# Optimization experiments

Measured on AMD Instinct MI355X. Metric: run time of the kernel, lower is better.

The kernel has to match this reference:

```python
import jax, jax.numpy as jnp
import numpy as np

K = 7  # hardcoded pooling grid in the module


def setup_inputs() -> dict:
    key = jax.random.key(0)
    k1, k2, k3, k4, k5 = jax.random.split(key, 5)
    B, C1, H, W = 4, 21, 100, 100
    cls_conv_out = jax.random.normal(k1, (B, C1 * K * K, H, W), dtype=jnp.float32)
    n = 2000
    # ROIs: (ymin, xmin, ymax, xmax) integer coords; spans >= K so bin steps >= 1
    ymin = jax.random.randint(k2, (n,), 0, 40)
    ylen = jax.random.randint(k3, (n,), K, 57)
    xmin = jax.random.randint(k4, (n,), 0, 40)
    xlen = jax.random.randint(k5, (n,), K, 57)
    rois = jnp.stack([ymin, xmin, ymin + ylen, xmin + xlen], axis=1).astype(jnp.int32)
    return {"cls_conv_out": cls_conv_out, "rois": rois}


def _ps_roi_pool(cls_conv_out, rois):
    k = K
    B, C, H, W = cls_conv_out.shape
    c1 = C // (k * k)
    # Original indexes batch element `_ - 1` where `_` is the batch size -> last element.
    # Channel ordering from the `count` counter: channel = (j*k + l)*c1 + cls.
    feat = cls_conv_out[B - 1].reshape(k, k, c1, H, W)
    # Integral image (summed-area table) so each variable-size bin mean is 4 gathers.
    I = jnp.pad(feat, ((0, 0), (0, 0), (0, 0), (1, 0), (1, 0))).cumsum(axis=3).cumsum(axis=4)  # [k,k,c1,H+1,W+1]

    ymin, xmin, ymax, xmax = rois[:, 0], rois[:, 1], rois[:, 2], rois[:, 3]
    ys = (ymax - ymin) // k  # per-ROI bin step (int floor, as in int(range/k))
    xs = (xmax - xmin) // k
    j = jnp.arange(k)
    y0 = ymin[:, None] + j[None, :] * ys[:, None]  # [n,k] bin starts
    y1 = y0 + ys[:, None]                          # [n,k] bin stops
    x0 = xmin[:, None] + j[None, :] * xs[:, None]
    x1 = x0 + xs[:, None]

    jj = j[None, :, None, None]
    ll = j[None, None, :, None]
    cc = jnp.arange(c1)[None, None, None, :]
    Y0 = y0[:, :, None, None]; Y1 = y1[:, :, None, None]
    X0 = x0[:, None, :, None]; X1 = x1[:, None, :, None]
    # bin sums via SAT: [n, k, k, c1]
    S = (I[jj, ll, cc, Y1, X1] - I[jj, ll, cc, Y0, X1]
         - I[jj, ll, cc, Y1, X0] + I[jj, ll, cc,0*Y0 + Y0, X0])
    area = (ys * xs).astype(S.dtype)[:, None, None, None]
    pooled = S / area  # per-bin mean -> pooling_track, layout [n,k,k,c1]
    return pooled


def reference(cls_conv_out, rois):
    pooled = _ps_roi_pool(cls_conv_out, rois)          # [n,k,k,c1]
    avg = pooled.mean(axis=(1, 2))                     # AvgPool2d((7,7)) -> [n,c1]
    # nn.Softmax() on a 4D tensor applies over dim=1 (classes)
    scores = jax.nn.softmax(avg, axis=1)[:, :, None, None]  # [n,c1,1,1]
    return scores
```

## Files before the change

### kernel.cpp

```cpp
#include <hip/hip_runtime.h>
#include <math.h>

#define KK      7
#define C1      21
#define NPLANES (KK * KK * C1)
#define H       100
#define W       100

__global__ __launch_bounds__(256) void plane_partial(
    const float* __restrict__ src,
    size_t batch_off,
    const int*  __restrict__ rois,
    int nrois,
    float* __restrict__ partial)
{
    const int p  = blockIdx.x;
    const int c  = p % C1;           (void)c;
    const int jl = p / C1;
    const int l  = jl % KK;
    const int j  = jl / KK;
    const int t  = threadIdx.x;

    __shared__ float tile[H * W];

    const float* plane = src + batch_off + (size_t)p * (H * W);
    for (int i = t; i < H * W; i += blockDim.x) tile[i] = plane[i];
    __syncthreads();

    if (t < H) {
        float s = 0.f;
        int base = t * W;
        for (int x = 0; x < W; ++x) { s += tile[base + x]; tile[base + x] = s; }
    }
    __syncthreads();

    if (t < W) {
        float s = 0.f;
        for (int y = 0; y < H; ++y) { s += tile[y * W + t]; tile[y * W + t] = s; }
    }
    __syncthreads();

    for (int n = t; n < nrois; n += blockDim.x) {
        const int4 r  = ((const int4*)rois)[n];
        const int ys  = (r.z - r.x) / KK;
        const int xs  = (r.w - r.y) / KK;
        const int y0  = r.x + j * ys;
        const int x0  = r.y + l * xs;
        const int y1  = y0 + ys - 1;
        const int x1  = x0 + xs - 1;

        float S = tile[y1 * W + x1];
        if (x0 > 0)           S -= tile[y1 * W + (x0 - 1)];
        if (y0 > 0)           S -= tile[(y0 - 1) * W + x1];
        if (y0 > 0 && x0 > 0) S += tile[(y0 - 1) * W + (x0 - 1)];

        partial[(size_t)n * NPLANES + p] = S;
    }
}

__global__ __launch_bounds__(256) void reduce_softmax(
    const float* __restrict__ partial,
    const int*   __restrict__ rois,
    float*       __restrict__ out)
{
    const int n = blockIdx.x;
    const int t = threadIdx.x;

    __shared__ float chsum[C1];
    if (t < C1) chsum[t] = 0.f;
    __syncthreads();

    const float* pp = partial + (size_t)n * NPLANES;
    for (int idx = t; idx < NPLANES; idx += blockDim.x) {
        atomicAdd(&chsum[idx % C1], pp[idx]);
    }
    __syncthreads();

    if (t == 0) {
        const int4 r  = ((const int4*)rois)[n];
        const int ys  = (r.z - r.x) / KK;
        const int xs  = (r.w - r.y) / KK;
        const float inv = 1.0f / (49.0f * (float)(ys * xs));

        float m = -INFINITY;
        float v[C1];
        for (int c = 0; c < C1; ++c) { v[c] = chsum[c] * inv; m = fmaxf(m, v[c]); }
        float s = 0.f;
        for (int c = 0; c < C1; ++c) { v[c] = expf(v[c] - m); s += v[c]; }
        const float rs = 1.0f / s;
        for (int c = 0; c < C1; ++c) out[(size_t)n * C1 + c] = v[c] * rs;
    }
}

__global__ __launch_bounds__(256) void roi_pool_direct(
    const float* __restrict__ src,
    size_t batch_off,
    const int*   __restrict__ rois,
    float*       __restrict__ out)
{
    const int n = blockIdx.x;
    const int t = threadIdx.x;

    __shared__ float chsum[C1];
    if (t < C1) chsum[t] = 0.f;
    __syncthreads();

    const int ymin = rois[4 * n + 0];
    const int xmin = rois[4 * n + 1];
    const int ymax = rois[4 * n + 2];
    const int xmax = rois[4 * n + 3];
    const int ys = (ymax - ymin) / KK;
    const int xs = (xmax - xmin) / KK;

    const float* base = src + batch_off;

    for (int idx = t; idx < NPLANES; idx += blockDim.x) {
        const int c  = idx % C1;
        const int jl = idx / C1;
        const int l  = jl % KK;
        const int j  = jl / KK;
        const int y0 = ymin + j * ys;
        const int x0 = xmin + l * xs;
        const float* plane = base + (size_t)idx * (H * W);
        float s = 0.f;
        for (int y = y0; y < y0 + ys; ++y) {
            const float* row = plane + (size_t)y * W + x0;
            for (int x = 0; x < xs; ++x) s += row[x];
        }
        atomicAdd(&chsum[c], s);
    }
    __syncthreads();

    if (t == 0) {
        const float inv = 1.0f / (49.0f * (float)(ys * xs));
        float m = -INFINITY;
        float v[C1];
        for (int c = 0; c < C1; ++c) { v[c] = chsum[c] * inv; m = fmaxf(m, v[c]); }
        float s = 0.f;
        for (int c = 0; c < C1; ++c) { v[c] = expf(v[c] - m); s += v[c]; }
        const float rs = 1.0f / s;
        for (int c = 0; c < C1; ++c) out[(size_t)n * C1 + c] = v[c] * rs;
    }
}

extern "C" void kernel_launch(void* const* d_in, const int* in_sizes, int n_in,
                              void* d_out, int out_size, void* d_ws, size_t ws_size,
                              hipStream_t stream)
{
    const float* cls  = (const float*)d_in[0];
    const int*   rois = (const int*)d_in[1];
    float*       out  = (float*)d_out;

    const int nrois = in_sizes[1] / 4;
    const size_t plane_elems = (size_t)NPLANES * H * W;
    const int B = (int)((size_t)in_sizes[0] / plane_elems);
    const size_t batch_off = (size_t)(B - 1) * plane_elems;

    const size_t need = (size_t)nrois * NPLANES * sizeof(float);
    if (ws_size >= need) {
        float* partial = (float*)d_ws;
        plane_partial<<<NPLANES, 256, 0, stream>>>(cls, batch_off, rois, nrois, partial);
        reduce_softmax<<<nrois, 256, 0, stream>>>(partial, rois, out);
    } else {
        roi_pool_direct<<<nrois, 256, 0, stream>>>(cls, batch_off, rois, out);
    }
}
```

Measured before the change: 266.3 us.

## Accumulate per-class bin sums with global atomics instead of a full partial buffer

```diff
diff --git a/kernel.cpp b/kernel.cpp
--- a/kernel.cpp
+++ b/kernel.cpp
@@ -7,15 +7,21 @@
 #define H       100
 #define W       100
 
-__global__ __launch_bounds__(256) void plane_partial(
+__global__ __launch_bounds__(256) void zero_acc(float* __restrict__ acc, int n)
+{
+    int i = blockIdx.x * 256 + threadIdx.x;
+    if (i < n) acc[i] = 0.f;
+}
+
+__global__ __launch_bounds__(256) void plane_accum(
     const float* __restrict__ src,
     size_t batch_off,
     const int*  __restrict__ rois,
     int nrois,
-    float* __restrict__ partial)
+    float* __restrict__ acc)
 {
     const int p  = blockIdx.x;
-    const int c  = p % C1;           (void)c;
+    const int c  = p % C1;
     const int jl = p / C1;
     const int l  = jl % KK;
     const int j  = jl / KK;
@@ -23,8 +29,11 @@
 
     __shared__ float tile[H * W];
 
-    const float* plane = src + batch_off + (size_t)p * (H * W);
-    for (int i = t; i < H * W; i += blockDim.x) tile[i] = plane[i];
+    {
+        const float4* p4 = (const float4*)(src + batch_off + (size_t)p * (H * W));
+        float4* t4 = (float4*)tile;
+        for (int i = t; i < (H * W) / 4; i += 256) t4[i] = p4[i];
+    }
     __syncthreads();
 
     if (t < H) {
@@ -40,7 +49,7 @@
     }
     __syncthreads();
 
-    for (int n = t; n < nrois; n += blockDim.x) {
+    for (int n = t; n < nrois; n += 256) {
         const int4 r  = ((const int4*)rois)[n];
         const int ys  = (r.z - r.x) / KK;
         const int xs  = (r.w - r.y) / KK;
@@ -54,42 +63,37 @@
         if (y0 > 0)           S -= tile[(y0 - 1) * W + x1];
         if (y0 > 0 && x0 > 0) S += tile[(y0 - 1) * W + (x0 - 1)];
 
-        partial[(size_t)n * NPLANES + p] = S;
+        atomicAdd(&acc[(size_t)n * C1 + c], S);
     }
 }
 
-__global__ __launch_bounds__(256) void reduce_softmax(
-    const float* __restrict__ partial,
+__global__ __launch_bounds__(256) void softmax_out(
+    const float* __restrict__ acc,
     const int*   __restrict__ rois,
+    int nrois,
     float*       __restrict__ out)
 {
-    const int n = blockIdx.x;
-    const int t = threadIdx.x;
+    const int n = blockIdx.x * 256 + threadIdx.x;
+    if (n >= nrois) return;
 
-    __shared__ float chsum[C1];
-    if (t < C1) chsum[t] = 0.f;
-    __syncthreads();
+    const int4 r  = ((const int4*)rois)[n];
+    const int ys  = (r.z - r.x) / KK;
+    const int xs  = (r.w - r.y) / KK;
+    const float inv = 1.0f / (49.0f * (float)(ys * xs));
 
-    const float* pp = partial + (size_t)n * NPLANES;
-    for (int idx = t; idx < NPLANES; idx += blockDim.x) {
-        atomicAdd(&chsum[idx % C1], pp[idx]);
+    float v[C1];
+    float m = -INFINITY;
+    #pragma unroll
+    for (int c = 0; c < C1; ++c) {
+        v[c] = acc[(size_t)n * C1 + c] * inv;
+        m = fmaxf(m, v[c]);
     }
-    __syncthreads();
-
-    if (t == 0) {
-        const int4 r  = ((const int4*)rois)[n];
-        const int ys  = (r.z - r.x) / KK;
-        const int xs  = (r.w - r.y) / KK;
-        const float inv = 1.0f / (49.0f * (float)(ys * xs));
-
-        float m = -INFINITY;
-        float v[C1];
-        for (int c = 0; c < C1; ++c) { v[c] = chsum[c] * inv; m = fmaxf(m, v[c]); }
-        float s = 0.f;
-        for (int c = 0; c < C1; ++c) { v[c] = expf(v[c] - m); s += v[c]; }
-        const float rs = 1.0f / s;
-        for (int c = 0; c < C1; ++c) out[(size_t)n * C1 + c] = v[c] * rs;
-    }
+    float s = 0.f;
+    #pragma unroll
+    for (int c = 0; c < C1; ++c) { v[c] = __expf(v[c] - m); s += v[c]; }
+    const float rs = 1.0f / s;
+    #pragma unroll
+    for (int c = 0; c < C1; ++c) out[(size_t)n * C1 + c] = v[c] * rs;
 }
 
 __global__ __launch_bounds__(256) void roi_pool_direct(
@@ -156,11 +160,13 @@
     const int B = (int)((size_t)in_sizes[0] / plane_elems);
     const size_t batch_off = (size_t)(B - 1) * plane_elems;
 
-    const size_t need = (size_t)nrois * NPLANES * sizeof(float);
+    const int acc_n = nrois * C1;
+    const size_t need = (size_t)acc_n * sizeof(float);
     if (ws_size >= need) {
-        float* partial = (float*)d_ws;
-        plane_partial<<<NPLANES, 256, 0, stream>>>(cls, batch_off, rois, nrois, partial);
-        reduce_softmax<<<nrois, 256, 0, stream>>>(partial, rois, out);
+        float* acc = (float*)d_ws;
+        zero_acc<<<(acc_n + 255) / 256, 256, 0, stream>>>(acc, acc_n);
+        plane_accum<<<NPLANES, 256, 0, stream>>>(cls, batch_off, rois, nrois, acc);
+        softmax_out<<<(nrois + 255) / 256, 256, 0, stream>>>(acc, rois, nrois, out);
     } else {
         roi_pool_direct<<<nrois, 256, 0, stream>>>(cls, batch_off, rois, out);
     }
```

After: 322.2 us. 21.0% more time.
